# Performance work log

Measured on AMD Instinct MI355X. Metric: run time of the kernel, lower is better.

Reference implementation:

```python
import jax, jax.numpy as jnp
import numpy as np

B, U, F = 8, 512, 64   # batch, universe points, fuzzy sets per rule
R = 256                # number of active rules


def setup_inputs() -> dict:
    key = jax.random.key(0)
    k1, k2 = jax.random.split(key)
    # fuzzy membership degrees in [0, 1]
    x = jax.random.uniform(k1, (B, U, F), dtype=jnp.float32)
    # active rules matrix (row r selects/weights fuzzy sets of rule r)
    active_rules = jax.random.uniform(k2, (R, F), dtype=jnp.float32)
    epoch = 1  # eval-mode style: rules are fixed, relation_algorithm not re-run
    return {"x": x, "active_rules": active_rules, "epoch": epoch}


def reference(x, active_rules, epoch):
    # relate_fuzzy_numbers: rules_per_universe[b,u,r,f] = x[b,u,f] * rules[r,f]
    # (original does this with nested Python loops over b and u; here one broadcast)
    rel = x[:, :, None, :] * active_rules[None, None, :, :]  # [B,U,R,F]
    # larsen intersection = product t-norm over the fuzzy-set dim (keepdim),
    # followed by x[:, :, :, 0] in forward -> plain product reduction.
    out = jnp.prod(rel, axis=-1)  # [B,U,R]
    return out
```

## Files before the change

kernel.cpp:

```cpp
#include <hip/hip_runtime.h>

#define BU   4096
#define F_   64
#define R_   256
#define ROWS_PER_BLOCK 16

__device__ __forceinline__ float d2f_ftz(double d) {
    return (d >= 0x1.0p-126) ? (float)d : 0.0f;
}

__global__ __launch_bounds__(256) void rules_outer_kernel(
        const float* __restrict__ x,
        const float* __restrict__ rules,
        float* __restrict__ out)
{
    __shared__ double sPr[R_];
    __shared__ double sPx[ROWS_PER_BLOCK];

    const int t   = threadIdx.x;
    const int bu0 = blockIdx.x * ROWS_PER_BLOCK;

    {
        const float4* rp = (const float4*)(rules + t * F_);
        double p = 1.0;
        #pragma unroll
        for (int i = 0; i < F_ / 4; ++i) {
            float4 v = rp[i];
            p *= (double)v.x; p *= (double)v.y;
            p *= (double)v.z; p *= (double)v.w;
        }
        sPr[t] = p;
    }

    if (t < ROWS_PER_BLOCK) {
        const float4* xp = (const float4*)(x + (size_t)(bu0 + t) * F_);
        double q = 1.0;
        #pragma unroll
        for (int i = 0; i < F_ / 4; ++i) {
            float4 v = xp[i];
            q *= (double)v.x; q *= (double)v.y;
            q *= (double)v.z; q *= (double)v.w;
        }
        sPx[t] = q;
    }
    __syncthreads();

    const int c    = t & 63;
    const int rowl = t >> 6;
    const int r0   = c * 4;

    const double pr0 = sPr[r0 + 0];
    const double pr1 = sPr[r0 + 1];
    const double pr2 = sPr[r0 + 2];
    const double pr3 = sPr[r0 + 3];

    #pragma unroll
    for (int pass = 0; pass < 4; ++pass) {
        const int row = pass * 4 + rowl;
        const double px = sPx[row];
        float4 o;
        o.x = d2f_ftz(px * pr0);
        o.y = d2f_ftz(px * pr1);
        o.z = d2f_ftz(px * pr2);
        o.w = d2f_ftz(px * pr3);
        *(float4*)(out + (size_t)(bu0 + row) * R_ + r0) = o;
    }
}

extern "C" void kernel_launch(void* const* d_in, const int* in_sizes, int n_in,
                              void* d_out, int out_size, void* d_ws, size_t ws_size,
                              hipStream_t stream) {
    const float* x     = (const float*)d_in[0];
    const float* rules = (const float*)d_in[1];
    float* out = (float*)d_out;

    rules_outer_kernel<<<BU / ROWS_PER_BLOCK, 256, 0, stream>>>(x, rules, out);
}
```

Baseline: 61.24 us.

## Split rule and x-row products across a 512-thread block with shuffle reduction

```diff
diff --git a/kernel.cpp b/kernel.cpp
--- a/kernel.cpp
+++ b/kernel.cpp
@@ -3,67 +3,65 @@
 #define BU   4096
 #define F_   64
 #define R_   256
-#define ROWS_PER_BLOCK 16
+#define ROWS 16
 
 __device__ __forceinline__ float d2f_ftz(double d) {
     return (d >= 0x1.0p-126) ? (float)d : 0.0f;
 }
 
-__global__ __launch_bounds__(256) void rules_outer_kernel(
+__global__ __launch_bounds__(512) void rules_outer_kernel(
         const float* __restrict__ x,
         const float* __restrict__ rules,
         float* __restrict__ out)
 {
     __shared__ double sPr[R_];
-    __shared__ double sPx[ROWS_PER_BLOCK];
+    __shared__ double sPx[ROWS];
 
     const int t   = threadIdx.x;
-    const int bu0 = blockIdx.x * ROWS_PER_BLOCK;
+    const int bu0 = blockIdx.x * ROWS;
 
-    {
-        const float4* rp = (const float4*)(rules + t * F_);
-        double p = 1.0;
+    if (t < R_) {
+        const float4* rp = (const float4*)(rules + (size_t)t * F_);
+        double p0 = 1.0, p1 = 1.0, p2 = 1.0, p3 = 1.0;
         #pragma unroll
         for (int i = 0; i < F_ / 4; ++i) {
             float4 v = rp[i];
-            p *= (double)v.x; p *= (double)v.y;
-            p *= (double)v.z; p *= (double)v.w;
+            p0 *= (double)v.x;
+            p1 *= (double)v.y;
+            p2 *= (double)v.z;
+            p3 *= (double)v.w;
         }
-        sPr[t] = p;
-    }
-
-    if (t < ROWS_PER_BLOCK) {
-        const float4* xp = (const float4*)(x + (size_t)(bu0 + t) * F_);
-        double q = 1.0;
-        #pragma unroll
-        for (int i = 0; i < F_ / 4; ++i) {
-            float4 v = xp[i];
-            q *= (double)v.x; q *= (double)v.y;
-            q *= (double)v.z; q *= (double)v.w;
-        }
-        sPx[t] = q;
+        sPr[t] = (p0 * p1) * (p2 * p3);
+    } else {
+        const int s   = t - R_;
+        const int row = s >> 4;
+        const int q   = s & 15;
+        float4 v = ((const float4*)(x + (size_t)(bu0 + row) * F_))[q];
+        double p = ((double)v.x * (double)v.y) * ((double)v.z * (double)v.w);
+        p *= __shfl_xor(p, 1);
+        p *= __shfl_xor(p, 2);
+        p *= __shfl_xor(p, 4);
+        p *= __shfl_xor(p, 8);
+        if (q == 0) sPx[row] = p;
     }
     __syncthreads();
 
     const int c    = t & 63;
-    const int rowl = t >> 6;
-    const int r0   = c * 4;
-
-    const double pr0 = sPr[r0 + 0];
-    const double pr1 = sPr[r0 + 1];
-    const double pr2 = sPr[r0 + 2];
-    const double pr3 = sPr[r0 + 3];
+    const int wrow = t >> 6;
+    const double pr0 = sPr[c];
+    const double pr1 = sPr[c + 64];
+    const double pr2 = sPr[c + 128];
+    const double pr3 = sPr[c + 192];
 
     #pragma unroll
-    for (int pass = 0; pass < 4; ++pass) {
-        const int row = pass * 4 + rowl;
+    for (int pass = 0; pass < 2; ++pass) {
+        const int row = wrow + pass * 8;
         const double px = sPx[row];
-        float4 o;
-        o.x = d2f_ftz(px * pr0);
-        o.y = d2f_ftz(px * pr1);
-        o.z = d2f_ftz(px * pr2);
-        o.w = d2f_ftz(px * pr3);
-        *(float4*)(out + (size_t)(bu0 + row) * R_ + r0) = o;
+        float* op = out + (size_t)(bu0 + row) * R_ + c;
+        op[0]   = d2f_ftz(px * pr0);
+        op[64]  = d2f_ftz(px * pr1);
+        op[128] = d2f_ftz(px * pr2);
+        op[192] = d2f_ftz(px * pr3);
     }
 }
 
@@ -74,5 +72,5 @@
     const float* rules = (const float*)d_in[1];
     float* out = (float*)d_out;
 
-    rules_outer_kernel<<<BU / ROWS_PER_BLOCK, 256, 0, stream>>>(x, rules, out);
+    rules_outer_kernel<<<BU / ROWS, 512, 0, stream>>>(x, rules, out);
 }
```

After: 59.87 us. 1.02x faster.
